# Performance work log

Hardware: AMD Instinct MI355X
Metric: run time of the kernel (lower is better)

The kernel has to match this reference:

```python
import jax, jax.numpy as jnp
import numpy as np

N, IN_DIM, OUT_DIM = 8192, 256, 64
NEG_INF = -9e15
SLOPE = 0.2


def setup_inputs() -> dict:
    key = jax.random.key(0)
    k1, k2, k3, k4 = jax.random.split(key, 4)
    h = jax.random.normal(k1, (N, IN_DIM), dtype=jnp.float32)
    adj = jax.random.randint(k2, (N, N), 0, 2, dtype=jnp.int32)
    W = jax.random.normal(k3, (IN_DIM, OUT_DIM), dtype=jnp.float32) * (1.0 / np.sqrt(IN_DIM))
    a = jax.random.normal(k4, (2 * OUT_DIM,), dtype=jnp.float32) * (1.0 / np.sqrt(2 * OUT_DIM))
    return {"h": h, "adj": adj, "W": W, "a": a}


def reference(h, adj, W, a):
    # Wh: [N, F]
    Wh = h @ W
    F = Wh.shape[-1]
    # a([Wh_i ; Wh_j]) decomposes: score_ij = a_left.Wh_i + a_right.Wh_j
    f_i = Wh @ a[:F]          # [N]
    f_j = Wh @ a[F:]          # [N]
    e = f_i[:, None] + f_j[None, :]            # [N, N] broadcast sum
    e = jnp.where(e >= 0, e, SLOPE * e)         # leaky relu (0.2)
    e = jnp.where(adj > 0, e, jnp.float32(NEG_INF))
    alpha = jax.nn.softmax(e, axis=1)           # row softmax over neighbors j
    return alpha @ Wh                            # [N, F]
```

## Files before the change

kernel.cpp:

```cpp
#include <hip/hip_runtime.h>
#include <hip/hip_fp16.h>

#define NN 8192
#define KDIM 256
#define FDIM 64
#define CBLK 1024
#define NSEG (NN / CBLK)

typedef __attribute__((ext_vector_type(8))) _Float16 f16x8;
typedef __attribute__((ext_vector_type(4))) float f32x4;
typedef __attribute__((ext_vector_type(4))) int i32x4;

union H2U { __half2 h; unsigned u; };
union HU  { __half h; unsigned short u; };

__device__ __forceinline__ unsigned h2u(__half2 h) { H2U x; x.h = h; return x.u; }

__device__ __forceinline__ unsigned pkmul(unsigned a, unsigned b) {
    unsigned d; asm("v_pk_mul_f16 %0, %1, %2" : "=v"(d) : "v"(a), "v"(b)); return d;
}
__device__ __forceinline__ unsigned pkmax(unsigned a, unsigned b) {
    unsigned d; asm("v_pk_max_f16 %0, %1, %2" : "=v"(d) : "v"(a), "v"(b)); return d;
}

__device__ __forceinline__ float wred64(float v) {
    v += __shfl_xor(v, 1);
    v += __shfl_xor(v, 2);
    v += __shfl_xor(v, 4);
    v += __shfl_xor(v, 8);
    v += __shfl_xor(v, 16);
    v += __shfl_xor(v, 32);
    return v;
}

__global__ __launch_bounds__(256) void gat_phase1(
    const float* __restrict__ h, const float* __restrict__ W,
    const float* __restrict__ a, unsigned short* __restrict__ wfrag,
    float* __restrict__ fi, float* __restrict__ fj)
{
    __shared__ unsigned short wht_s[FDIM][20];
    const int tid = threadIdx.x;
    const int f  = tid & 63;
    const int rg = tid >> 6;
    const int i0 = blockIdx.x << 4;

    const float* __restrict__ h0 = h + (size_t)(i0 + rg * 4) * KDIM;
    const float* __restrict__ h1 = h0 + KDIM;
    const float* __restrict__ h2 = h0 + 2 * KDIM;
    const float* __restrict__ h3 = h0 + 3 * KDIM;

    float acc0 = 0.f, acc1 = 0.f, acc2 = 0.f, acc3 = 0.f;
    #pragma unroll 4
    for (int k4 = 0; k4 < KDIM / 4; ++k4) {
        const float4 r0 = *(const float4*)(h0 + k4 * 4);
        const float4 r1 = *(const float4*)(h1 + k4 * 4);
        const float4 r2 = *(const float4*)(h2 + k4 * 4);
        const float4 r3 = *(const float4*)(h3 + k4 * 4);
        const float w0 = W[(k4 * 4 + 0) * FDIM + f];
        const float w1 = W[(k4 * 4 + 1) * FDIM + f];
        const float w2 = W[(k4 * 4 + 2) * FDIM + f];
        const float w3 = W[(k4 * 4 + 3) * FDIM + f];
        acc0 += r0.x * w0 + r0.y * w1 + r0.z * w2 + r0.w * w3;
        acc1 += r1.x * w0 + r1.y * w1 + r1.z * w2 + r1.w * w3;
        acc2 += r2.x * w0 + r2.y * w1 + r2.z * w2 + r2.w * w3;
        acc3 += r3.x * w0 + r3.y * w1 + r3.z * w2 + r3.w * w3;
    }

    HU c0; c0.h = __float2half(acc0);
    HU c1; c1.h = __float2half(acc1);
    HU c2; c2.h = __float2half(acc2);
    HU c3; c3.h = __float2half(acc3);
    const int r0i = rg * 4;
    wht_s[f][r0i + 0] = c0.u;
    wht_s[f][r0i + 1] = c1.u;
    wht_s[f][r0i + 2] = c2.u;
    wht_s[f][r0i + 3] = c3.u;

    const float aL = a[f];
    const float aR = a[FDIM + f];
    float s;
    s = wred64(acc0 * aL); if (f == 0) fi[i0 + r0i + 0] = s;
    s = wred64(acc1 * aL); if (f == 0) fi[i0 + r0i + 1] = s;
    s = wred64(acc2 * aL); if (f == 0) fi[i0 + r0i + 2] = s;
    s = wred64(acc3 * aL); if (f == 0) fi[i0 + r0i + 3] = s;
    s = wred64(acc0 * aR); if (f == 0) fj[i0 + r0i + 0] = s;
    s = wred64(acc1 * aR); if (f == 0) fj[i0 + r0i + 1] = s;
    s = wred64(acc2 * aR); if (f == 0) fj[i0 + r0i + 2] = s;
    s = wred64(acc3 * aR); if (f == 0) fj[i0 + r0i + 3] = s;

    __syncthreads();
    if (tid < 128) {
        const int li2 = tid & 15;
        const int q2  = (tid >> 4) & 1;
        const int b   = tid >> 5;
        const int t   = i0 >> 5;
        const int hh  = (i0 >> 4) & 1;
        const int feat = b * 16 + li2;
        const ushort4 lo = *(const ushort4*)&wht_s[feat][q2 * 8];
        const ushort4 hi = *(const ushort4*)&wht_s[feat][q2 * 8 + 4];
        const int lg = (hh * 2 + q2) * 16 + li2;
        unsigned short* dst = wfrag + (size_t)t * 2048 + b * 512 + lg * 8;
        *(ushort4*)(dst)     = lo;
        *(ushort4*)(dst + 4) = hi;
    }
}

__global__ __launch_bounds__(256, 4) void gat_fused(
    const int* __restrict__ adj, const unsigned short* __restrict__ wfrag,
    const float* __restrict__ fi, const float* __restrict__ fjg,
    float* __restrict__ vpart, float* __restrict__ zpart)
{
    __shared__ unsigned mask_lds[16][33];
    __shared__ unsigned Ebuf[1024];
    __shared__ float red[2 * 16 * 64];
    __shared__ float zred[4][16];

    const int tid = threadIdx.x;
    const int w  = tid >> 6;
    const int l  = tid & 63;
    const int li = l & 15;
    const int q  = l >> 4;
    const int qo = q * 8;
    const int bid = blockIdx.x;
    const int seg = bid & (NSEG - 1);
    const int i0  = (bid / NSEG) << 4;

    unsigned* E1p = Ebuf;
    unsigned* E2p = Ebuf + 512;
    for (int t = tid; t < 512; t += 256) {
        const float2 f2 = ((const float2*)fjg)[seg * 512 + t];
        E1p[t] = h2u(__floats2half2_rn(__expf(f2.x), __expf(f2.y)));
        E2p[t] = h2u(__floats2half2_rn(__expf(0.2f * f2.x), __expf(0.2f * f2.y)));
    }

    const int wsel = (l & 7) * 4;
    #pragma unroll
    for (int rp = 0; rp < 2; ++rp) {
        const int r0 = 4 * w + 2 * rp;
        const i32x4* __restrict__ p0 =
            (const i32x4*)(adj + (size_t)(i0 + r0) * NN + seg * CBLK);
        const i32x4* __restrict__ p1 = p0 + (NN / 4);
        i32x4 v[8];
        #pragma unroll
        for (int k = 0; k < 4; ++k) v[k]     = __builtin_nontemporal_load(&p0[k * 64 + l]);
        #pragma unroll
        for (int k = 0; k < 4; ++k) v[4 + k] = __builtin_nontemporal_load(&p1[k * 64 + l]);
        #pragma unroll
        for (int k = 0; k < 8; ++k) {
            const i32x4 x = v[k];
            unsigned nib = (unsigned)(x[0] > 0) | ((unsigned)(x[1] > 0) << 1)
                         | ((unsigned)(x[2] > 0) << 2) | ((unsigned)(x[3] > 0) << 3);
            unsigned p = nib << wsel;
            p |= __shfl_xor(p, 1);
            p |= __shfl_xor(p, 2);
            p |= __shfl_xor(p, 4);
            const int rr = r0 + (k >> 2);
            if ((l & 7) == 0) mask_lds[rr][(k & 3) * 8 + (l >> 3)] = p;
        }
    }

    const float fiv = fi[i0 + li];
    const unsigned e1i2 = h2u(__floats2half2_rn(__expf(fiv), __expf(fiv)));
    const unsigned e2i2 = h2u(__floats2half2_rn(__expf(0.2f * fiv), __expf(0.2f * fiv)));
    const unsigned short* __restrict__ wf =
        wfrag + (size_t)(seg * 32) * 2048 + l * 8;

    __syncthreads();

    f32x4 acc0 = {0.f, 0.f, 0.f, 0.f};
    f32x4 acc1 = {0.f, 0.f, 0.f, 0.f};
    f32x4 acc2 = {0.f, 0.f, 0.f, 0.f};
    f32x4 acc3 = {0.f, 0.f, 0.f, 0.f};
    f32x4 accz = {0.f, 0.f, 0.f, 0.f};
    const f16x8 ones = { (_Float16)1.f, (_Float16)1.f, (_Float16)1.f, (_Float16)1.f,
                         (_Float16)1.f, (_Float16)1.f, (_Float16)1.f, (_Float16)1.f };

    #pragma unroll 4
    for (int s = 0; s < 8; ++s) {
        const int tw = w + 4 * s;
        const unsigned mword = mask_lds[li][tw];
        const unsigned mq8 = (mword >> qo) & 0xFFu;
        const int ep = tw * 16 + q * 4;
        const uint4 e1w = *(const uint4*)(E1p + ep);
        const uint4 e2w = *(const uint4*)(E2p + ep);
        const unsigned short* wt = wf + (size_t)tw * 2048;
        const f16x8 b0 = *(const f16x8*)(wt);
        const f16x8 b1 = *(const f16x8*)(wt + 512);
        const f16x8 b2 = *(const f16x8*)(wt + 1024);
        const f16x8 b3 = *(const f16x8*)(wt + 1536);

        const unsigned mm0 = ((mq8 &   1u) ? 0x0000FFFFu : 0u) | ((mq8 &   2u) ? 0xFFFF0000u : 0u);
        const unsigned mm1 = ((mq8 &   4u) ? 0x0000FFFFu : 0u) | ((mq8 &   8u) ? 0xFFFF0000u : 0u);
        const unsigned mm2 = ((mq8 &  16u) ? 0x0000FFFFu : 0u) | ((mq8 &  32u) ? 0xFFFF0000u : 0u);
        const unsigned mm3 = ((mq8 &  64u) ? 0x0000FFFFu : 0u) | ((mq8 & 128u) ? 0xFFFF0000u : 0u);

        union { unsigned u[4]; f16x8 v; } af;
        af.u[0] = pkmax(pkmul(e1i2, e1w.x), pkmul(e2i2, e2w.x)) & mm0;
        af.u[1] = pkmax(pkmul(e1i2, e1w.y), pkmul(e2i2, e2w.y)) & mm1;
        af.u[2] = pkmax(pkmul(e1i2, e1w.z), pkmul(e2i2, e2w.z)) & mm2;
        af.u[3] = pkmax(pkmul(e1i2, e1w.w), pkmul(e2i2, e2w.w)) & mm3;

        acc0 = __builtin_amdgcn_mfma_f32_16x16x32_f16(af.v, b0, acc0, 0, 0, 0);
        acc1 = __builtin_amdgcn_mfma_f32_16x16x32_f16(af.v, b1, acc1, 0, 0, 0);
        acc2 = __builtin_amdgcn_mfma_f32_16x16x32_f16(af.v, b2, acc2, 0, 0, 0);
        acc3 = __builtin_amdgcn_mfma_f32_16x16x32_f16(af.v, b3, acc3, 0, 0, 0);
        accz = __builtin_amdgcn_mfma_f32_16x16x32_f16(af.v, ones, accz, 0, 0, 0);
    }

    if (li == 0) {
        #pragma unroll
        for (int r = 0; r < 4; ++r)
            zred[w][q * 4 + r] = accz[r];
    }
    if (w < 2) {
        #pragma unroll
        for (int r = 0; r < 4; ++r) {
            red[(w * 16 + q * 4 + r) * 64 + 0 * 16 + li] = acc0[r];
            red[(w * 16 + q * 4 + r) * 64 + 1 * 16 + li] = acc1[r];
            red[(w * 16 + q * 4 + r) * 64 + 2 * 16 + li] = acc2[r];
            red[(w * 16 + q * 4 + r) * 64 + 3 * 16 + li] = acc3[r];
        }
    }
    __syncthreads();
    if (w >= 2) {
        #pragma unroll
        for (int r = 0; r < 4; ++r) {
            red[((w - 2) * 16 + q * 4 + r) * 64 + 0 * 16 + li] += acc0[r];
            red[((w - 2) * 16 + q * 4 + r) * 64 + 1 * 16 + li] += acc1[r];
            red[((w - 2) * 16 + q * 4 + r) * 64 + 2 * 16 + li] += acc2[r];
            red[((w - 2) * 16 + q * 4 + r) * 64 + 3 * 16 + li] += acc3[r];
        }
    }
    __syncthreads();

    const int f  = tid & 63;
    const int ig = tid >> 6;
    #pragma unroll
    for (int cc = 0; cc < 4; ++cc) {
        const int i = cc * 4 + ig;
        const float v = red[(0 * 16 + i) * 64 + f] + red[(1 * 16 + i) * 64 + f];
        vpart[(size_t)(seg * NN + i0 + i) * FDIM + f] = v;
        if (f == 0) {
            const float zz = (zred[0][i] + zred[1][i]) + (zred[2][i] + zred[3][i]);
            zpart[seg * NN + i0 + i] = zz;
        }
    }
}

__global__ __launch_bounds__(256) void gat_merge(
    const float* __restrict__ vpart, const float* __restrict__ zpart,
    float* __restrict__ out)
{
    const int g = blockIdx.x * 256 + threadIdx.x;
    const int row = g >> 4;
    float4 v = ((const float4*)vpart)[g];
    float z = zpart[row];
    #pragma unroll
    for (int k = 1; k < NSEG; ++k) {
        const float4 b = ((const float4*)vpart)[g + (size_t)k * NN * (FDIM / 4)];
        v.x += b.x; v.y += b.y; v.z += b.z; v.w += b.w;
        z += zpart[row + k * NN];
    }
    float4 o;
    o.x = v.x / z; o.y = v.y / z; o.z = v.z / z; o.w = v.w / z;
    ((float4*)out)[g] = o;
}

extern "C" void kernel_launch(void* const* d_in, const int* in_sizes, int n_in,
                              void* d_out, int out_size, void* d_ws, size_t ws_size,
                              hipStream_t stream) {
    const float* h   = (const float*)d_in[0];
    const int*   adj = (const int*)d_in[1];
    const float* W   = (const float*)d_in[2];
    const float* a   = (const float*)d_in[3];
    float* out = (float*)d_out;

    unsigned short* wfrag = (unsigned short*)d_ws;
    float* fi = (float*)((char*)d_ws + (size_t)NN * FDIM * 2);
    float* fj = fi + NN;
    float* vpart = (float*)((char*)d_ws + (2u << 20));
    float* zpart = (float*)((char*)d_ws + (18u << 20));

    gat_phase1<<<NN / 16, 256, 0, stream>>>(h, W, a, wfrag, fi, fj);
    gat_fused<<<(NN / 16) * NSEG, 256, 0, stream>>>(adj, wfrag, fi, fj, vpart, zpart);
    gat_merge<<<NN * FDIM / 1024, 256, 0, stream>>>(vpart, zpart, out);
}
```

Baseline: 92.75 us.

## Warp-specialize fused GAT kernel with producer/consumer mask ring, drop merge pass

Each block now handles 16 full rows instead of one column segment. Four producer waves stream the adjacency rows into a 4-slot LDS ring of bitmasks, and four consumer waves run the MFMA accumulation, synchronised through LDS counters. Because each block sees the whole row, it normalises by the row sum and writes the output directly, which removes the partial-sum buffers and the separate merge kernel. In exchange the grid drops to 512 blocks of 512 threads, which may limit the memory parallelism available to stream adj. The spin-waits and the 32KB Ebuf per block may also reduce occupancy.

```diff
diff --git a/kernel.cpp b/kernel.cpp
--- a/kernel.cpp
+++ b/kernel.cpp
@@ -4,8 +4,8 @@
 #define NN 8192
 #define KDIM 256
 #define FDIM 64
-#define CBLK 1024
-#define NSEG (NN / CBLK)
+#define NCH 8
+#define NSLOT 4
 
 typedef __attribute__((ext_vector_type(8))) _Float16 f16x8;
 typedef __attribute__((ext_vector_type(4))) float f32x4;
@@ -105,14 +105,15 @@
     }
 }
 
-__global__ __launch_bounds__(256, 4) void gat_fused(
+__global__ __launch_bounds__(512, 4) void gat_fused(
     const int* __restrict__ adj, const unsigned short* __restrict__ wfrag,
     const float* __restrict__ fi, const float* __restrict__ fjg,
-    float* __restrict__ vpart, float* __restrict__ zpart)
+    float* __restrict__ out)
 {
-    __shared__ unsigned mask_lds[16][33];
-    __shared__ unsigned Ebuf[1024];
-    __shared__ float red[2 * 16 * 64];
+    __shared__ unsigned Ebuf[8192];
+    __shared__ unsigned ring[NSLOT][16][33];
+    __shared__ unsigned prod_cnt[NSLOT];
+    __shared__ unsigned cons_cnt[NSLOT];
     __shared__ float zred[4][16];
 
     const int tid = threadIdx.x;
@@ -121,50 +122,14 @@
     const int li = l & 15;
     const int q  = l >> 4;
     const int qo = q * 8;
-    const int bid = blockIdx.x;
-    const int seg = bid & (NSEG - 1);
-    const int i0  = (bid / NSEG) << 4;
-
-    unsigned* E1p = Ebuf;
-    unsigned* E2p = Ebuf + 512;
-    for (int t = tid; t < 512; t += 256) {
-        const float2 f2 = ((const float2*)fjg)[seg * 512 + t];
-        E1p[t] = h2u(__floats2half2_rn(__expf(f2.x), __expf(f2.y)));
-        E2p[t] = h2u(__floats2half2_rn(__expf(0.2f * f2.x), __expf(0.2f * f2.y)));
-    }
-
-    const int wsel = (l & 7) * 4;
-    #pragma unroll
-    for (int rp = 0; rp < 2; ++rp) {
-        const int r0 = 4 * w + 2 * rp;
-        const i32x4* __restrict__ p0 =
-            (const i32x4*)(adj + (size_t)(i0 + r0) * NN + seg * CBLK);
-        const i32x4* __restrict__ p1 = p0 + (NN / 4);
-        i32x4 v[8];
-        #pragma unroll
-        for (int k = 0; k < 4; ++k) v[k]     = __builtin_nontemporal_load(&p0[k * 64 + l]);
-        #pragma unroll
-        for (int k = 0; k < 4; ++k) v[4 + k] = __builtin_nontemporal_load(&p1[k * 64 + l]);
-        #pragma unroll
-        for (int k = 0; k < 8; ++k) {
-            const i32x4 x = v[k];
-            unsigned nib = (unsigned)(x[0] > 0) | ((unsigned)(x[1] > 0) << 1)
-                         | ((unsigned)(x[2] > 0) << 2) | ((unsigned)(x[3] > 0) << 3);
-            unsigned p = nib << wsel;
-            p |= __shfl_xor(p, 1);
-            p |= __shfl_xor(p, 2);
-            p |= __shfl_xor(p, 4);
-            const int rr = r0 + (k >> 2);
-            if ((l & 7) == 0) mask_lds[rr][(k & 3) * 8 + (l >> 3)] = p;
-        }
-    }
-
-    const float fiv = fi[i0 + li];
-    const unsigned e1i2 = h2u(__floats2half2_rn(__expf(fiv), __expf(fiv)));
-    const unsigned e2i2 = h2u(__floats2half2_rn(__expf(0.2f * fiv), __expf(0.2f * fiv)));
-    const unsigned short* __restrict__ wf =
-        wfrag + (size_t)(seg * 32) * 2048 + l * 8;
-
+    const int i0 = blockIdx.x << 4;
+
+    if (tid < NSLOT) { prod_cnt[tid] = 0; cons_cnt[tid] = 0; }
+    for (int t = tid; t < 4096; t += 512) {
+        const float2 f2 = ((const float2*)fjg)[t];
+        Ebuf[t]        = h2u(__floats2half2_rn(__expf(f2.x), __expf(f2.y)));
+        Ebuf[4096 + t] = h2u(__floats2half2_rn(__expf(0.2f * f2.x), __expf(0.2f * f2.y)));
+    }
     __syncthreads();
 
     f32x4 acc0 = {0.f, 0.f, 0.f, 0.f};
@@ -172,98 +137,144 @@
     f32x4 acc2 = {0.f, 0.f, 0.f, 0.f};
     f32x4 acc3 = {0.f, 0.f, 0.f, 0.f};
     f32x4 accz = {0.f, 0.f, 0.f, 0.f};
-    const f16x8 ones = { (_Float16)1.f, (_Float16)1.f, (_Float16)1.f, (_Float16)1.f,
-                         (_Float16)1.f, (_Float16)1.f, (_Float16)1.f, (_Float16)1.f };
-
-    #pragma unroll 4
-    for (int s = 0; s < 8; ++s) {
-        const int tw = w + 4 * s;
-        const unsigned mword = mask_lds[li][tw];
-        const unsigned mq8 = (mword >> qo) & 0xFFu;
-        const int ep = tw * 16 + q * 4;
-        const uint4 e1w = *(const uint4*)(E1p + ep);
-        const uint4 e2w = *(const uint4*)(E2p + ep);
-        const unsigned short* wt = wf + (size_t)tw * 2048;
-        const f16x8 b0 = *(const f16x8*)(wt);
-        const f16x8 b1 = *(const f16x8*)(wt + 512);
-        const f16x8 b2 = *(const f16x8*)(wt + 1024);
-        const f16x8 b3 = *(const f16x8*)(wt + 1536);
-
-        const unsigned mm0 = ((mq8 &   1u) ? 0x0000FFFFu : 0u) | ((mq8 &   2u) ? 0xFFFF0000u : 0u);
-        const unsigned mm1 = ((mq8 &   4u) ? 0x0000FFFFu : 0u) | ((mq8 &   8u) ? 0xFFFF0000u : 0u);
-        const unsigned mm2 = ((mq8 &  16u) ? 0x0000FFFFu : 0u) | ((mq8 &  32u) ? 0xFFFF0000u : 0u);
-        const unsigned mm3 = ((mq8 &  64u) ? 0x0000FFFFu : 0u) | ((mq8 & 128u) ? 0xFFFF0000u : 0u);
-
-        union { unsigned u[4]; f16x8 v; } af;
-        af.u[0] = pkmax(pkmul(e1i2, e1w.x), pkmul(e2i2, e2w.x)) & mm0;
-        af.u[1] = pkmax(pkmul(e1i2, e1w.y), pkmul(e2i2, e2w.y)) & mm1;
-        af.u[2] = pkmax(pkmul(e1i2, e1w.z), pkmul(e2i2, e2w.z)) & mm2;
-        af.u[3] = pkmax(pkmul(e1i2, e1w.w), pkmul(e2i2, e2w.w)) & mm3;
-
-        acc0 = __builtin_amdgcn_mfma_f32_16x16x32_f16(af.v, b0, acc0, 0, 0, 0);
-        acc1 = __builtin_amdgcn_mfma_f32_16x16x32_f16(af.v, b1, acc1, 0, 0, 0);
-        acc2 = __builtin_amdgcn_mfma_f32_16x16x32_f16(af.v, b2, acc2, 0, 0, 0);
-        acc3 = __builtin_amdgcn_mfma_f32_16x16x32_f16(af.v, b3, acc3, 0, 0, 0);
-        accz = __builtin_amdgcn_mfma_f32_16x16x32_f16(af.v, ones, accz, 0, 0, 0);
-    }
-
-    if (li == 0) {
-        #pragma unroll
-        for (int r = 0; r < 4; ++r)
-            zred[w][q * 4 + r] = accz[r];
-    }
-    if (w < 2) {
+
+    if (w < 4) {
+        const int p = w;
+        const int wsel = (l & 7) * 4;
+        #pragma unroll 1
+        for (int c = 0; c < NCH; ++c) {
+            const int s = c & (NSLOT - 1);
+            const unsigned gen = (unsigned)(c >> 2);
+            volatile unsigned* vcc = cons_cnt;
+            while (vcc[s] < 4u * gen) __builtin_amdgcn_s_sleep(1);
+            asm volatile("" ::: "memory");
+            #pragma unroll
+            for (int rp = 0; rp < 2; ++rp) {
+                i32x4 v[8];
+                #pragma unroll
+                for (int r = 0; r < 2; ++r) {
+                    const i32x4* rowp =
+                        (const i32x4*)(adj + (size_t)(i0 + 4 * p + 2 * rp + r) * NN + c * 1024);
+                    #pragma unroll
+                    for (int j = 0; j < 4; ++j)
+                        v[r * 4 + j] = __builtin_nontemporal_load(&rowp[j * 64 + l]);
+                }
+                #pragma unroll
+                for (int r = 0; r < 2; ++r)
+                #pragma unroll
+                for (int j = 0; j < 4; ++j) {
+                    const i32x4 x = v[r * 4 + j];
+                    unsigned nib = (unsigned)(x[0] > 0) | ((unsigned)(x[1] > 0) << 1)
+                                 | ((unsigned)(x[2] > 0) << 2) | ((unsigned)(x[3] > 0) << 3);
+                    unsigned pt = nib << wsel;
+                    pt |= __shfl_xor(pt, 1);
+                    pt |= __shfl_xor(pt, 2);
+                    pt |= __shfl_xor(pt, 4);
+                    if ((l & 7) == 0)
+                        ring[s][4 * p + 2 * rp + r][8 * j + (l >> 3)] = pt;
+                }
+            }
+            __threadfence_block();
+            if (l == 0) atomicAdd(&prod_cnt[s], 1u);
+        }
+    } else {
+        const int qw = w - 4;
+        const float fiv = fi[i0 + li];
+        const unsigned e1i2 = h2u(__floats2half2_rn(__expf(fiv), __expf(fiv)));
+        const unsigned e2i2 = h2u(__floats2half2_rn(__expf(0.2f * fiv), __expf(0.2f * fiv)));
+        const unsigned short* __restrict__ wf = wfrag + l * 8;
+        const unsigned* E1p = Ebuf;
+        const unsigned* E2p = Ebuf + 4096;
+        const f16x8 ones = { (_Float16)1.f, (_Float16)1.f, (_Float16)1.f, (_Float16)1.f,
+                             (_Float16)1.f, (_Float16)1.f, (_Float16)1.f, (_Float16)1.f };
+
+        #pragma unroll 1
+        for (int c = 0; c < NCH; ++c) {
+            const int s = c & (NSLOT - 1);
+            const unsigned need = 4u * (unsigned)((c >> 2) + 1);
+            volatile unsigned* vpc = prod_cnt;
+            while (vpc[s] < need) __builtin_amdgcn_s_sleep(1);
+            asm volatile("" ::: "memory");
+            #pragma unroll 2
+            for (int k = 0; k < 8; ++k) {
+                const int twl = qw + 4 * k;
+                const int gtw = c * 32 + twl;
+                const unsigned mword = ring[s][li][twl];
+                const unsigned mq8 = (mword >> qo) & 0xFFu;
+                const int ep = gtw * 16 + q * 4;
+                const uint4 e1w = *(const uint4*)(E1p + ep);
+                const uint4 e2w = *(const uint4*)(E2p + ep);
+                const unsigned short* wt = wf + (size_t)gtw * 2048;
+                const f16x8 b0 = *(const f16x8*)(wt);
+                const f16x8 b1 = *(const f16x8*)(wt + 512);
+                const f16x8 b2 = *(const f16x8*)(wt + 1024);
+                const f16x8 b3 = *(const f16x8*)(wt + 1536);
+
+                const unsigned mm0 = ((mq8 &   1u) ? 0x0000FFFFu : 0u) | ((mq8 &   2u) ? 0xFFFF0000u : 0u);
+                const unsigned mm1 = ((mq8 &   4u) ? 0x0000FFFFu : 0u) | ((mq8 &   8u) ? 0xFFFF0000u : 0u);
+                const unsigned mm2 = ((mq8 &  16u) ? 0x0000FFFFu : 0u) | ((mq8 &  32u) ? 0xFFFF0000u : 0u);
+                const unsigned mm3 = ((mq8 &  64u) ? 0x0000FFFFu : 0u) | ((mq8 & 128u) ? 0xFFFF0000u : 0u);
+
+                union { unsigned u[4]; f16x8 v; } af;
+                af.u[0] = pkmax(pkmul(e1i2, e1w.x), pkmul(e2i2, e2w.x)) & mm0;
+                af.u[1] = pkmax(pkmul(e1i2, e1w.y), pkmul(e2i2, e2w.y)) & mm1;
+                af.u[2] = pkmax(pkmul(e1i2, e1w.z), pkmul(e2i2, e2w.z)) & mm2;
+                af.u[3] = pkmax(pkmul(e1i2, e1w.w), pkmul(e2i2, e2w.w)) & mm3;
+
+                acc0 = __builtin_amdgcn_mfma_f32_16x16x32_f16(af.v, b0, acc0, 0, 0, 0);
+                acc1 = __builtin_amdgcn_mfma_f32_16x16x32_f16(af.v, b1, acc1, 0, 0, 0);
+                acc2 = __builtin_amdgcn_mfma_f32_16x16x32_f16(af.v, b2, acc2, 0, 0, 0);
+                acc3 = __builtin_amdgcn_mfma_f32_16x16x32_f16(af.v, b3, acc3, 0, 0, 0);
+                accz = __builtin_amdgcn_mfma_f32_16x16x32_f16(af.v, ones, accz, 0, 0, 0);
+            }
+            asm volatile("" ::: "memory");
+            if (l == 0) atomicAdd(&cons_cnt[s], 1u);
+        }
+    }
+
+    __syncthreads();
+    float* red = (float*)Ebuf;
+    if (w >= 4) {
+        const int qw = w - 4;
+        if (li == 0) {
+            #pragma unroll
+            for (int r = 0; r < 4; ++r)
+                zred[qw][q * 4 + r] = accz[r];
+        }
+        if (qw < 2) {
+            #pragma unroll
+            for (int r = 0; r < 4; ++r) {
+                red[(qw * 16 + q * 4 + r) * 64 + 0 * 16 + li] = acc0[r];
+                red[(qw * 16 + q * 4 + r) * 64 + 1 * 16 + li] = acc1[r];
+                red[(qw * 16 + q * 4 + r) * 64 + 2 * 16 + li] = acc2[r];
+                red[(qw * 16 + q * 4 + r) * 64 + 3 * 16 + li] = acc3[r];
+            }
+        }
+    }
+    __syncthreads();
+    if (w >= 6) {
+        const int qw = w - 6;
         #pragma unroll
         for (int r = 0; r < 4; ++r) {
-            red[(w * 16 + q * 4 + r) * 64 + 0 * 16 + li] = acc0[r];
-            red[(w * 16 + q * 4 + r) * 64 + 1 * 16 + li] = acc1[r];
-            red[(w * 16 + q * 4 + r) * 64 + 2 * 16 + li] = acc2[r];
-            red[(w * 16 + q * 4 + r) * 64 + 3 * 16 + li] = acc3[r];
-        }
-    }
-    __syncthreads();
-    if (w >= 2) {
+            red[(qw * 16 + q * 4 + r) * 64 + 0 * 16 + li] += acc0[r];
+            red[(qw * 16 + q * 4 + r) * 64 + 1 * 16 + li] += acc1[r];
+            red[(qw * 16 + q * 4 + r) * 64 + 2 * 16 + li] += acc2[r];
+            red[(qw * 16 + q * 4 + r) * 64 + 3 * 16 + li] += acc3[r];
+        }
+    }
+    __syncthreads();
+
+    if (tid < 256) {
+        const int f  = tid & 63;
+        const int ig = tid >> 6;
         #pragma unroll
-        for (int r = 0; r < 4; ++r) {
-            red[((w - 2) * 16 + q * 4 + r) * 64 + 0 * 16 + li] += acc0[r];
-            red[((w - 2) * 16 + q * 4 + r) * 64 + 1 * 16 + li] += acc1[r];
-            red[((w - 2) * 16 + q * 4 + r) * 64 + 2 * 16 + li] += acc2[r];
-            red[((w - 2) * 16 + q * 4 + r) * 64 + 3 * 16 + li] += acc3[r];
-        }
-    }
-    __syncthreads();
-
-    const int f  = tid & 63;
-    const int ig = tid >> 6;
-    #pragma unroll
-    for (int cc = 0; cc < 4; ++cc) {
-        const int i = cc * 4 + ig;
-        const float v = red[(0 * 16 + i) * 64 + f] + red[(1 * 16 + i) * 64 + f];
-        vpart[(size_t)(seg * NN + i0 + i) * FDIM + f] = v;
-        if (f == 0) {
-            const float zz = (zred[0][i] + zred[1][i]) + (zred[2][i] + zred[3][i]);
-            zpart[seg * NN + i0 + i] = zz;
-        }
-    }
-}
-
-__global__ __launch_bounds__(256) void gat_merge(
-    const float* __restrict__ vpart, const float* __restrict__ zpart,
-    float* __restrict__ out)
-{
-    const int g = blockIdx.x * 256 + threadIdx.x;
-    const int row = g >> 4;
-    float4 v = ((const float4*)vpart)[g];
-    float z = zpart[row];
-    #pragma unroll
-    for (int k = 1; k < NSEG; ++k) {
-        const float4 b = ((const float4*)vpart)[g + (size_t)k * NN * (FDIM / 4)];
-        v.x += b.x; v.y += b.y; v.z += b.z; v.w += b.w;
-        z += zpart[row + k * NN];
-    }
-    float4 o;
-    o.x = v.x / z; o.y = v.y / z; o.z = v.z / z; o.w = v.w / z;
-    ((float4*)out)[g] = o;
+        for (int cc = 0; cc < 4; ++cc) {
+            const int i = cc * 4 + ig;
+            const float v = red[(0 * 16 + i) * 64 + f] + red[(1 * 16 + i) * 64 + f];
+            const float z = (zred[0][i] + zred[1][i]) + (zred[2][i] + zred[3][i]);
+            out[(size_t)(i0 + i) * FDIM + f] = v / z;
+        }
+    }
 }
 
 extern "C" void kernel_launch(void* const* d_in, const int* in_sizes, int n_in,
@@ -278,10 +289,7 @@
     unsigned short* wfrag = (unsigned short*)d_ws;
     float* fi = (float*)((char*)d_ws + (size_t)NN * FDIM * 2);
     float* fj = fi + NN;
-    float* vpart = (float*)((char*)d_ws + (2u << 20));
-    float* zpart = (float*)((char*)d_ws + (18u << 20));
 
     gat_phase1<<<NN / 16, 256, 0, stream>>>(h, W, a, wfrag, fi, fj);
-    gat_fused<<<(NN / 16) * NSEG, 256, 0, stream>>>(adj, wfrag, fi, fj, vpart, zpart);
-    gat_merge<<<NN * FDIM / 1024, 256, 0, stream>>>(vpart, zpart, out);
-}
+    gat_fused<<<NN / 16, 512, 0, stream>>>(adj, wfrag, fi, fj, out);
+}
```

Result: slower. 109.7 us (+18.2%).
